# Kernel optimization log

Hardware: AMD Instinct MI355X
Metric: run time of the kernel (lower is better)

## Reference

```python
import jax, jax.numpy as jnp
import numpy as np

V, E, H, D = 30000, 300, 300, 300   # vocab, embed, enc_hid, dec_hid
B, TL, AL, QL = 128, 400, 50, 32    # batch, text_len, answer_len, question_len


def setup_inputs() -> dict:
    key = jax.random.key(0)
    ks = iter(jax.random.split(key, 40))
    def p(shape):
        return jax.random.normal(next(ks), shape, jnp.float32) * 0.05
    inp = {
        'text': jax.random.randint(next(ks), (B, TL), 0, V),
        'answer': jax.random.randint(next(ks), (B, AL), 0, V),
        'question': jax.random.randint(next(ks), (B, QL), 0, V),
        'embedding': p((V, E)),
        # text encoder (bidirectional GRU), torch gate order r,z,n
        'te_Wih_f': p((E, 3 * H)), 'te_Whh_f': p((H, 3 * H)), 'te_bih_f': p((3 * H,)), 'te_bhh_f': p((3 * H,)),
        'te_Wih_b': p((E, 3 * H)), 'te_Whh_b': p((H, 3 * H)), 'te_bih_b': p((3 * H,)), 'te_bhh_b': p((3 * H,)),
        # answer encoder (bidirectional GRU)
        'ae_Wih_f': p((E, 3 * H)), 'ae_Whh_f': p((H, 3 * H)), 'ae_bih_f': p((3 * H,)), 'ae_bhh_f': p((3 * H,)),
        'ae_Wih_b': p((E, 3 * H)), 'ae_Whh_b': p((H, 3 * H)), 'ae_bih_b': p((3 * H,)), 'ae_bhh_b': p((3 * H,)),
        'trans_W': p((2 * H, D)), 'trans_b': p((D,)),
        # attention: Linear(2H+D, D) split into key(D) and query(2H) blocks (cat order: key, queries)
        'attn_Wk': p((D, D)), 'attn_Wq': p((2 * H, D)), 'attn_b': p((D,)),
        'attn_v': jax.random.uniform(next(ks), (D,), jnp.float32),
        # decoder GRU cell, input = [emb(E), weighted(2H)]
        'dec_Wih': p((E + 2 * H, 3 * D)), 'dec_Whh': p((D, 3 * D)), 'dec_bih': p((3 * D,)), 'dec_bhh': p((3 * D,)),
        'out_W': p((D + 2 * H + E, V)), 'out_b': p((V,)),
    }
    return inp


def gru_cell(x, h, Wih, Whh, bih, bhh):
    gi = x @ Wih + bih
    gh = h @ Whh + bhh
    ir, iz, inn = jnp.split(gi, 3, axis=-1)
    hr, hz, hn = jnp.split(gh, 3, axis=-1)
    r = jax.nn.sigmoid(ir + hr)
    z = jax.nn.sigmoid(iz + hz)
    n = jnp.tanh(inn + r * hn)
    return (1 - z) * n + z * h


def gru_seq(x, Wih, Whh, bih, bhh, reverse=False):
    # x: [B,T,in] -> [B,T,H]
    xt = jnp.swapaxes(x, 0, 1)
    h0 = jnp.zeros((x.shape[0], Whh.shape[0]), x.dtype)
    def step(h, xt_):
        h = gru_cell(xt_, h, Wih, Whh, bih, bhh)
        return h, h
    _, ys = jax.lax.scan(step, h0, xt, reverse=reverse)
    return jnp.swapaxes(ys, 0, 1)


def bigru(x, Wih_f, Whh_f, bih_f, bhh_f, Wih_b, Whh_b, bih_b, bhh_b):
    fwd = gru_seq(x, Wih_f, Whh_f, bih_f, bhh_f, reverse=False)
    bwd = gru_seq(x, Wih_b, Whh_b, bih_b, bhh_b, reverse=True)
    return jnp.concatenate([fwd, bwd], axis=-1)  # [B,T,2H]


def reference(text, answer, question, embedding,
              te_Wih_f, te_Whh_f, te_bih_f, te_bhh_f, te_Wih_b, te_Whh_b, te_bih_b, te_bhh_b,
              ae_Wih_f, ae_Whh_f, ae_bih_f, ae_bhh_f, ae_Wih_b, ae_Whh_b, ae_bih_b, ae_bhh_b,
              trans_W, trans_b, attn_Wk, attn_Wq, attn_b, attn_v,
              dec_Wih, dec_Whh, dec_bih, dec_bhh, out_W, out_b):
    text_emb = embedding[text]          # [B,TL,E] (eval: dropout off)
    ans_emb = embedding[answer]
    q_emb = embedding[question]         # [B,QL,E]

    text_rep = bigru(text_emb, te_Wih_f, te_Whh_f, te_bih_f, te_bhh_f,
                     te_Wih_b, te_Whh_b, te_bih_b, te_bhh_b)      # [B,TL,2H]
    ans_rep = bigru(ans_emb, ae_Wih_f, ae_Whh_f, ae_bih_f, ae_bhh_f,
                    ae_Wih_b, ae_Whh_b, ae_bih_b, ae_bhh_b)       # [B,AL,2H]

    hidden0 = ans_rep[:, -1, :] @ trans_W + trans_b               # [B,D]
    # precompute query projection of attention (invariant over decode steps)
    qproj = jnp.einsum('bse,ed->bsd', text_rep, attn_Wq) + attn_b  # [B,TL,D]

    def step(h, emb_t):  # emb_t: [B,E]
        energy = jnp.tanh(qproj + (h @ attn_Wk)[:, None, :])      # [B,TL,D]
        scores = jnp.einsum('bsd,d->bs', energy, attn_v)
        a = jax.nn.softmax(scores, axis=1)
        weighted = jnp.einsum('bs,bse->be', a, text_rep)           # [B,2H]
        rnn_in = jnp.concatenate([emb_t, weighted], axis=-1)
        h_new = gru_cell(rnn_in, h, dec_Wih, dec_Whh, dec_bih, dec_bhh)
        logits = jnp.concatenate([h_new, weighted, emb_t], axis=-1) @ out_W + out_b
        return h_new, logits

    emb_seq = jnp.swapaxes(q_emb[:, :-1], 0, 1)  # teacher forcing: input at t is question[t-1]
    _, logits = jax.lax.scan(step, hidden0, emb_seq)   # [QL-1,B,V]
    logits = jnp.swapaxes(logits, 0, 1)                # [B,QL-1,V]
    outputs = jnp.concatenate([jnp.zeros((logits.shape[0], 1, logits.shape[2]), logits.dtype), logits], axis=1)
    return outputs  # [B,QL,V]
```

## Files before the change

### kernel.cpp

```cpp
#include <hip/hip_runtime.h>
#include <hip/hip_bf16.h>
#include <stdint.h>

typedef unsigned short u16;
typedef __attribute__((ext_vector_type(8))) short short8;
typedef __attribute__((ext_vector_type(4))) float f32x4;

#define B_   128
#define TL_  400
#define AL_  50
#define QL_  32
#define E_   300
#define H3_  900
#define V_   30000
#define EP_  320
#define K2P_ 640
#define KDP_ 1216
#define NDP_ 1920
#define MT_  51200
#define MA_  6400
#define MD_  3968

static __device__ __forceinline__ float bf2f(u16 u) {
    union { float f; unsigned v; } c; c.v = ((unsigned)u) << 16; return c.f;
}
static __device__ __forceinline__ u16 f2bf(float f) {
    union { float f; unsigned v; } c; c.f = f;
    unsigned r = c.v + 0x7FFF + ((c.v >> 16) & 1);
    return (u16)(r >> 16);
}
static __device__ __forceinline__ float sigm(float x) { return 1.f / (1.f + __expf(-x)); }

__global__ __launch_bounds__(256) void transpose_cvt(const float* __restrict__ src, int K, int N,
                                                     u16* __restrict__ dst, int ldbt, int n0, int k0) {
    __shared__ float tile[32][33];
    int kb = blockIdx.x * 32, nb = blockIdx.y * 32;
    int tx = threadIdx.x & 31, ty = threadIdx.x >> 5;
    for (int i = ty; i < 32; i += 8) {
        int k = kb + i, n = nb + tx;
        tile[i][tx] = (k < K && n < N) ? src[(size_t)k * N + n] : 0.f;
    }
    __syncthreads();
    for (int i = ty; i < 32; i += 8) {
        int n = nb + i, k = kb + tx;
        if (n < N && k < K) dst[(size_t)(n0 + n) * ldbt + k0 + k] = f2bf(tile[tx][i]);
    }
}

__global__ __launch_bounds__(256) void build_dec_bias(const float* __restrict__ bih,
                                                      const float* __restrict__ bhh,
                                                      float* __restrict__ bias) {
    int i = blockIdx.x * 256 + threadIdx.x;
    if (i < 900) bias[i] = bih[i];
    else if (i < 1800) bias[i] = bhh[i - 900];
    else if (i < NDP_) bias[i] = 0.f;
}

__global__ __launch_bounds__(256) void gather_rows(const int* __restrict__ idx, const float* __restrict__ emb,
                                                   u16* __restrict__ dst, int ldd) {
    int r = blockIdx.x;
    int id = idx[r];
    const float* e = emb + (size_t)id * E_;
    for (int i = threadIdx.x; i < E_; i += 256) dst[(size_t)r * ldd + i] = f2bf(e[i]);
}

__global__ __launch_bounds__(256) void gather_q(const int* __restrict__ question, const float* __restrict__ emb,
                                                u16* __restrict__ A_dec, u16* __restrict__ A_out) {
    int r = blockIdx.x;
    int t = r >> 7, b = r & 127;
    int id = question[b * QL_ + t];
    const float* e = emb + (size_t)id * E_;
    for (int i = threadIdx.x; i < E_; i += 256) {
        u16 u = f2bf(e[i]);
        A_dec[(size_t)r * KDP_ + i] = u;
        A_out[(size_t)r * KDP_ + 900 + i] = u;
    }
}

template <int MODE>
__global__ __launch_bounds__(256) void gemm_bt(const u16* __restrict__ A, int lda,
                                               const u16* __restrict__ Bt, int ldb,
                                               void* __restrict__ Cv, int ldc, int Nreal,
                                               const float* __restrict__ bias, int Kpad) {
    __shared__ u16 lA[128 * 32];
    __shared__ u16 lB[128 * 32];
    const int tid = threadIdx.x;
    const int bn = blockIdx.x, bm = blockIdx.y;
    const long row0 = (long)bm * 128;
    const u16* Ab = A + row0 * lda;
    const u16* Bb = Bt + (long)bn * 128 * ldb;
    const int lane = tid & 63, wave = tid >> 6;
    const int wr = wave >> 1, wc = wave & 1;
    const int lr = lane & 15, ko = (lane >> 4) * 8;
    f32x4 acc[4][4] = {};

    for (int k0 = 0; k0 < Kpad; k0 += 32) {
#pragma unroll
        for (int i = 0; i < 2; ++i) {
            const int c = tid + 256 * i;
            const int e = c * 8;
            const int r = e >> 5, col = e & 31;
            __builtin_amdgcn_global_load_lds(
                (const __attribute__((address_space(1))) void*)(Ab + (long)r * lda + k0 + col),
                (__attribute__((address_space(3))) void*)(&lA[e]), 16, 0, 0);
            __builtin_amdgcn_global_load_lds(
                (const __attribute__((address_space(1))) void*)(Bb + (long)r * ldb + k0 + col),
                (__attribute__((address_space(3))) void*)(&lB[e]), 16, 0, 0);
        }
        __syncthreads();
        short8 af[4], bfr[4];
#pragma unroll
        for (int i = 0; i < 4; ++i) {
            af[i]  = *(const short8*)&lA[(wr * 64 + i * 16 + lr) * 32 + ko];
            bfr[i] = *(const short8*)&lB[(wc * 64 + i * 16 + lr) * 32 + ko];
        }
#pragma unroll
        for (int i = 0; i < 4; ++i)
#pragma unroll
            for (int j = 0; j < 4; ++j)
                acc[i][j] = __builtin_amdgcn_mfma_f32_16x16x32_bf16(af[i], bfr[j], acc[i][j], 0, 0, 0);
        __syncthreads();
    }

    const int r4 = (lane >> 4) * 4;
    const int cl = lane & 15;
#pragma unroll
    for (int i = 0; i < 4; ++i) {
#pragma unroll
        for (int j = 0; j < 4; ++j) {
            const int colg = bn * 128 + wc * 64 + j * 16 + cl;
            if (colg >= Nreal) continue;
            const float bv = bias ? bias[colg] : 0.f;
#pragma unroll
            for (int v = 0; v < 4; ++v) {
                const long rowg = row0 + wr * 64 + i * 16 + r4 + v;
                const float val = acc[i][j][v] + bv;
                if (MODE == 0) {
                    ((float*)Cv)[rowg * (long)ldc + colg] = val;
                } else if (MODE == 1) {
                    ((u16*)Cv)[rowg * (long)ldc + colg] = f2bf(val);
                } else {
                    const int tt = (int)(rowg >> 7), bb = (int)(rowg & 127);
                    ((float*)Cv)[((long)bb * QL_ + tt + 1) * (long)V_ + colg] = val;
                }
            }
        }
    }
}

__global__ __launch_bounds__(256) void enc_step(int t,
        const float* __restrict__ Whh_tf, const float* __restrict__ Whh_tb,
        const float* __restrict__ Whh_af, const float* __restrict__ Whh_ab,
        const float* __restrict__ bhh_tf, const float* __restrict__ bhh_tb,
        const float* __restrict__ bhh_af, const float* __restrict__ bhh_ab,
        const u16* __restrict__ gi_tf, const u16* __restrict__ gi_tb,
        const u16* __restrict__ gi_af, const u16* __restrict__ gi_ab,
        float* __restrict__ h_enc, u16* __restrict__ text_rep) {
    const int blk = blockIdx.x;
    const int task = blk / 80;
    const int bg = (blk % 80) / 5;
    const int jc = blk % 5;
    if (task == 2 && t >= AL_) return;
    if (task == 3 && t != 0) return;
    const float* Whh; const float* bhh; const u16* gi; int T;
    if (task == 0)      { Whh = Whh_tf; bhh = bhh_tf; gi = gi_tf; T = TL_; }
    else if (task == 1) { Whh = Whh_tb; bhh = bhh_tb; gi = gi_tb; T = TL_; }
    else if (task == 2) { Whh = Whh_af; bhh = bhh_af; gi = gi_af; T = AL_; }
    else                { Whh = Whh_ab; bhh = bhh_ab; gi = gi_ab; T = AL_; }
    const int t_eff = (task == 1 || task == 3) ? (T - 1 - t) : t;

    __shared__ float hs[8 * 300];
    const float* h_cur = h_enc + (size_t)(((t & 1) * 4 + task) * 128 + bg * 8) * 300;
    float* h_nxt = h_enc + (size_t)((((t + 1) & 1) * 4 + task) * 128) * 300;
    const int tid = threadIdx.x;
    for (int i = tid; i < 2400; i += 256) hs[i] = h_cur[i];
    __syncthreads();

    const int j = jc * 64 + (tid & 63);
    if (j >= 300) return;
    const int bs = tid >> 6;
    float a0r = 0, a0z = 0, a0n = 0, a1r = 0, a1z = 0, a1n = 0;
    for (int k = 0; k < 300; ++k) {
        const float* wrow = Whh + k * 900;
        const float w0 = wrow[j], w1 = wrow[j + 300], w2 = wrow[j + 600];
        const float h0 = hs[bs * 300 + k], h1 = hs[(bs + 4) * 300 + k];
        a0r += h0 * w0; a0z += h0 * w1; a0n += h0 * w2;
        a1r += h1 * w0; a1z += h1 * w1; a1n += h1 * w2;
    }
    const float br = bhh[j], bz = bhh[j + 300], bnn = bhh[j + 600];
#pragma unroll
    for (int half = 0; half < 2; ++half) {
        const int bl = bs + half * 4;
        const int b = bg * 8 + bl;
        const float gr_ = half ? a1r : a0r, gz_ = half ? a1z : a0z, gn_ = half ? a1n : a0n;
        const size_t gidx = ((size_t)b * T + t_eff) * 900;
        const float gir = bf2f(gi[gidx + j]);
        const float giz = bf2f(gi[gidx + j + 300]);
        const float gin = bf2f(gi[gidx + j + 600]);
        const float r = sigm(gir + gr_ + br);
        const float z = sigm(giz + gz_ + bz);
        const float n = tanhf(gin + r * (gn_ + bnn));
        const float hp = hs[bl * 300 + j];
        const float hn = (1.f - z) * n + z * hp;
        h_nxt[(size_t)b * 300 + j] = hn;
        if (task < 2) text_rep[((size_t)b * TL_ + t_eff) * K2P_ + task * 300 + j] = f2bf(hn);
    }
}

__global__ __launch_bounds__(256) void trans_hidden(const float* __restrict__ h_enc,
                                                    const float* __restrict__ trans_W,
                                                    const float* __restrict__ trans_b,
                                                    float* __restrict__ h_dec, u16* __restrict__ A_dec0) {
    int b = blockIdx.x, tid = threadIdx.x;
    __shared__ float si[600];
    const float* af = h_enc + (size_t)((0 * 4 + 2) * 128 + b) * 300;
    const float* ab = h_enc + (size_t)((1 * 4 + 3) * 128 + b) * 300;
    for (int i = tid; i < 300; i += 256) { si[i] = af[i]; si[300 + i] = ab[i]; }
    __syncthreads();
    for (int jj = tid; jj < 300; jj += 256) {
        float acc = trans_b[jj];
        for (int k = 0; k < 600; ++k) acc += si[k] * trans_W[k * 300 + jj];
        h_dec[(size_t)b * 300 + jj] = acc;
        A_dec0[(size_t)b * KDP_ + 900 + jj] = f2bf(acc);
    }
}

__global__ __launch_bounds__(256) void attn_step(int t, const float* __restrict__ h_dec,
                                                 const float* __restrict__ Wk, const float* __restrict__ av,
                                                 const float* __restrict__ qproj, const u16* __restrict__ text_rep,
                                                 u16* __restrict__ A_dec_t, u16* __restrict__ A_out) {
    const int b = blockIdx.x, tid = threadIdx.x, lane = tid & 63, wave = tid >> 6;
    __shared__ float sh[300], hwk[300], sc[400], red[8];
    for (int i = tid; i < 300; i += 256) sh[i] = h_dec[(size_t)b * 300 + i];
    __syncthreads();
    for (int jj = tid; jj < 300; jj += 256) {
        float acc = 0.f;
        for (int k = 0; k < 300; ++k) acc += sh[k] * Wk[k * 300 + jj];
        hwk[jj] = acc;
    }
    __syncthreads();
    for (int s = wave; s < 400; s += 4) {
        const float* qp = qproj + ((size_t)b * TL_ + s) * 300;
        float p = 0.f;
        for (int d = lane; d < 300; d += 64) {
            float e = qp[d] + hwk[d];
            e = fminf(fmaxf(e, -15.f), 15.f);
            float ex = __expf(2.f * e);
            p += ((ex - 1.f) / (ex + 1.f)) * av[d];
        }
#pragma unroll
        for (int off = 32; off > 0; off >>= 1) p += __shfl_down(p, off);
        if (lane == 0) sc[s] = p;
    }
    __syncthreads();
    float m = -1e30f;
    for (int i = tid; i < 400; i += 256) m = fmaxf(m, sc[i]);
#pragma unroll
    for (int off = 32; off > 0; off >>= 1) m = fmaxf(m, __shfl_down(m, off));
    if (lane == 0) red[wave] = m;
    __syncthreads();
    m = fmaxf(fmaxf(red[0], red[1]), fmaxf(red[2], red[3]));
    float ssum = 0.f;
    for (int i = tid; i < 400; i += 256) { float e = __expf(sc[i] - m); sc[i] = e; ssum += e; }
#pragma unroll
    for (int off = 32; off > 0; off >>= 1) ssum += __shfl_down(ssum, off);
    if (lane == 0) red[4 + wave] = ssum;
    __syncthreads();
    const float inv = 1.f / (red[4] + red[5] + red[6] + red[7]);
    for (int e0 = tid; e0 < 600; e0 += 256) {
        float acc = 0.f;
        for (int s = 0; s < 400; ++s) acc += sc[s] * bf2f(text_rep[((size_t)b * TL_ + s) * K2P_ + e0]);
        u16 wv = f2bf(acc * inv);
        A_dec_t[(size_t)b * KDP_ + 300 + e0] = wv;
        A_out[((size_t)t * 128 + b) * KDP_ + 300 + e0] = wv;
    }
}

__global__ __launch_bounds__(256) void dec_gate(int t, const float* __restrict__ g_all,
                                                float* __restrict__ h_dec,
                                                u16* __restrict__ A_dec, u16* __restrict__ A_out) {
    int idx = blockIdx.x * 256 + threadIdx.x;
    if (idx >= 128 * 300) return;
    int b = idx / 300, j = idx % 300;
    const float* g = g_all + (size_t)b * NDP_;
    float r = sigm(g[j] + g[900 + j]);
    float z = sigm(g[300 + j] + g[1200 + j]);
    float n = tanhf(g[600 + j] + r * g[1500 + j]);
    float hp = h_dec[idx];
    float hn = (1.f - z) * n + z * hp;
    h_dec[idx] = hn;
    u16 u = f2bf(hn);
    A_out[((size_t)t * 128 + b) * KDP_ + j] = u;
    if (t < 30) A_dec[((size_t)(t + 1) * 128 + b) * KDP_ + 900 + j] = u;
}

__global__ __launch_bounds__(256) void zero_t0(float* __restrict__ out) {
    int i = blockIdx.x * 256 + threadIdx.x;
    if (i < 128 * V_) {
        int b = i / V_, v = i % V_;
        out[(size_t)b * QL_ * V_ + v] = 0.f;
    }
}

extern "C" void kernel_launch(void* const* d_in, const int* in_sizes, int n_in,
                              void* d_out, int out_size, void* d_ws, size_t ws_size,
                              hipStream_t stream) {
    (void)in_sizes; (void)n_in; (void)out_size;
    const int*   text      = (const int*)d_in[0];
    const int*   answer    = (const int*)d_in[1];
    const int*   question  = (const int*)d_in[2];
    const float* embedding = (const float*)d_in[3];
    const float* te_Wih_f = (const float*)d_in[4],  *te_Whh_f = (const float*)d_in[5];
    const float* te_bih_f = (const float*)d_in[6],  *te_bhh_f = (const float*)d_in[7];
    const float* te_Wih_b = (const float*)d_in[8],  *te_Whh_b = (const float*)d_in[9];
    const float* te_bih_b = (const float*)d_in[10], *te_bhh_b = (const float*)d_in[11];
    const float* ae_Wih_f = (const float*)d_in[12], *ae_Whh_f = (const float*)d_in[13];
    const float* ae_bih_f = (const float*)d_in[14], *ae_bhh_f = (const float*)d_in[15];
    const float* ae_Wih_b = (const float*)d_in[16], *ae_Whh_b = (const float*)d_in[17];
    const float* ae_bih_b = (const float*)d_in[18], *ae_bhh_b = (const float*)d_in[19];
    const float* trans_W  = (const float*)d_in[20], *trans_b  = (const float*)d_in[21];
    const float* attn_Wk  = (const float*)d_in[22], *attn_Wq  = (const float*)d_in[23];
    const float* attn_b   = (const float*)d_in[24], *attn_v   = (const float*)d_in[25];
    const float* dec_Wih  = (const float*)d_in[26], *dec_Whh  = (const float*)d_in[27];
    const float* dec_bih  = (const float*)d_in[28], *dec_bhh  = (const float*)d_in[29];
    const float* out_W    = (const float*)d_in[30], *out_b    = (const float*)d_in[31];
    float* out = (float*)d_out;

    char* w = (char*)d_ws; size_t off = 0;
    auto alloc = [&](size_t bytes) -> void* { void* p = w + off; off += (bytes + 255) & ~(size_t)255; return p; };
    u16* WihT_tf = (u16*)alloc(1024 * EP_ * 2);
    u16* WihT_tb = (u16*)alloc(1024 * EP_ * 2);
    u16* WihT_af = (u16*)alloc(1024 * EP_ * 2);
    u16* WihT_ab = (u16*)alloc(1024 * EP_ * 2);
    u16* WqT     = (u16*)alloc(384 * K2P_ * 2);
    u16* outWT   = (u16*)alloc((size_t)30080 * KDP_ * 2);
    u16* decBT   = (u16*)alloc((size_t)NDP_ * KDP_ * 2);
    float* decBias = (float*)alloc(NDP_ * 4);
    u16* textEmb = (u16*)alloc((size_t)MT_ * EP_ * 2);
    u16* ansEmb  = (u16*)alloc((size_t)MA_ * EP_ * 2);
    u16* gi_tf   = (u16*)alloc((size_t)MT_ * 900 * 2);
    u16* gi_tb   = (u16*)alloc((size_t)MT_ * 900 * 2);
    u16* gi_af   = (u16*)alloc((size_t)MA_ * 900 * 2);
    u16* gi_ab   = (u16*)alloc((size_t)MA_ * 900 * 2);
    u16* text_rep = (u16*)alloc((size_t)MT_ * K2P_ * 2);
    float* qproj = (float*)alloc((size_t)MT_ * 300 * 4);
    float* h_enc = (float*)alloc((size_t)2 * 4 * 128 * 300 * 4);
    float* h_dec = (float*)alloc((size_t)128 * 300 * 4);
    u16* A_dec   = (u16*)alloc((size_t)MD_ * KDP_ * 2);
    u16* A_out   = (u16*)alloc((size_t)MD_ * KDP_ * 2);
    float* gi_gh = (float*)alloc((size_t)128 * NDP_ * 4);
    const size_t need = off;
    size_t zbytes = need <= ws_size ? need : ws_size;

    hipMemsetAsync(d_ws, 0, zbytes, stream);

    transpose_cvt<<<dim3(10, 29), 256, 0, stream>>>(te_Wih_f, 300, 900, WihT_tf, EP_, 0, 0);
    transpose_cvt<<<dim3(10, 29), 256, 0, stream>>>(te_Wih_b, 300, 900, WihT_tb, EP_, 0, 0);
    transpose_cvt<<<dim3(10, 29), 256, 0, stream>>>(ae_Wih_f, 300, 900, WihT_af, EP_, 0, 0);
    transpose_cvt<<<dim3(10, 29), 256, 0, stream>>>(ae_Wih_b, 300, 900, WihT_ab, EP_, 0, 0);
    transpose_cvt<<<dim3(19, 10), 256, 0, stream>>>(attn_Wq, 600, 300, WqT, K2P_, 0, 0);
    transpose_cvt<<<dim3(38, 938), 256, 0, stream>>>(out_W, 1200, V_, outWT, KDP_, 0, 0);
    transpose_cvt<<<dim3(29, 29), 256, 0, stream>>>(dec_Wih, 900, 900, decBT, KDP_, 0, 0);
    transpose_cvt<<<dim3(10, 29), 256, 0, stream>>>(dec_Whh, 300, 900, decBT, KDP_, 900, 900);
    build_dec_bias<<<8, 256, 0, stream>>>(dec_bih, dec_bhh, decBias);

    gather_rows<<<MT_, 256, 0, stream>>>(text, embedding, textEmb, EP_);
    gather_rows<<<MA_, 256, 0, stream>>>(answer, embedding, ansEmb, EP_);
    gather_q<<<MD_, 256, 0, stream>>>(question, embedding, A_dec, A_out);

    gemm_bt<1><<<dim3(8, 400), 256, 0, stream>>>(textEmb, EP_, WihT_tf, EP_, gi_tf, 900, 900, te_bih_f, EP_);
    gemm_bt<1><<<dim3(8, 400), 256, 0, stream>>>(textEmb, EP_, WihT_tb, EP_, gi_tb, 900, 900, te_bih_b, EP_);
    gemm_bt<1><<<dim3(8, 50),  256, 0, stream>>>(ansEmb, EP_, WihT_af, EP_, gi_af, 900, 900, ae_bih_f, EP_);
    gemm_bt<1><<<dim3(8, 50),  256, 0, stream>>>(ansEmb, EP_, WihT_ab, EP_, gi_ab, 900, 900, ae_bih_b, EP_);

    for (int t = 0; t < TL_; ++t)
        enc_step<<<320, 256, 0, stream>>>(t, te_Whh_f, te_Whh_b, ae_Whh_f, ae_Whh_b,
                                          te_bhh_f, te_bhh_b, ae_bhh_f, ae_bhh_b,
                                          gi_tf, gi_tb, gi_af, gi_ab, h_enc, text_rep);

    trans_hidden<<<128, 256, 0, stream>>>(h_enc, trans_W, trans_b, h_dec, A_dec);
    gemm_bt<0><<<dim3(3, 400), 256, 0, stream>>>(text_rep, K2P_, WqT, K2P_, qproj, 300, 300, attn_b, K2P_);

    for (int t = 0; t < QL_ - 1; ++t) {
        attn_step<<<128, 256, 0, stream>>>(t, h_dec, attn_Wk, attn_v, qproj, text_rep,
                                           A_dec + (size_t)t * 128 * KDP_, A_out);
        gemm_bt<0><<<dim3(15, 1), 256, 0, stream>>>(A_dec + (size_t)t * 128 * KDP_, KDP_,
                                                    decBT, KDP_, gi_gh, NDP_, 1800, decBias, KDP_);
        dec_gate<<<150, 256, 0, stream>>>(t, gi_gh, h_dec, A_dec, A_out);
    }

    gemm_bt<2><<<dim3(235, 31), 256, 0, stream>>>(A_out, KDP_, outWT, KDP_, d_out, 0, V_, out_b, KDP_);
    zero_t0<<<(128 * V_ + 255) / 256, 256, 0, stream>>>(out);
}
```

Before: 18.73 ms.

## Replace per-step encoder GRU launches with persistent MFMA kernel over time

```diff
diff --git a/kernel.cpp b/kernel.cpp
--- a/kernel.cpp
+++ b/kernel.cpp
@@ -4,6 +4,7 @@
 
 typedef unsigned short u16;
 typedef __attribute__((ext_vector_type(8))) short short8;
+typedef __attribute__((ext_vector_type(8))) _Float16 half8;
 typedef __attribute__((ext_vector_type(4))) float f32x4;
 
 #define B_   128
@@ -11,7 +12,6 @@
 #define AL_  50
 #define QL_  32
 #define E_   300
-#define H3_  900
 #define V_   30000
 #define EP_  320
 #define K2P_ 640
@@ -20,6 +20,7 @@
 #define MT_  51200
 #define MA_  6400
 #define MD_  3968
+#define WPT_ (10*1024*32)
 
 static __device__ __forceinline__ float bf2f(u16 u) {
     union { float f; unsigned v; } c; c.v = ((unsigned)u) << 16; return c.f;
@@ -28,6 +29,9 @@
     union { float f; unsigned v; } c; c.f = f;
     unsigned r = c.v + 0x7FFF + ((c.v >> 16) & 1);
     return (u16)(r >> 16);
+}
+static __device__ __forceinline__ u16 f2h_bits(float f) {
+    _Float16 h = (_Float16)f; u16 u; __builtin_memcpy(&u, &h, 2); return u;
 }
 static __device__ __forceinline__ float sigm(float x) { return 1.f / (1.f + __expf(-x)); }
 
@@ -45,6 +49,26 @@
         int n = nb + i, k = kb + tx;
         if (n < N && k < K) dst[(size_t)(n0 + n) * ldbt + k0 + k] = f2bf(tile[tx][i]);
     }
+}
+
+__global__ __launch_bounds__(320) void prep_whh(const float* __restrict__ W0, const float* __restrict__ W1,
+                                                const float* __restrict__ W2, const float* __restrict__ W3,
+                                                const float* __restrict__ b0, const float* __restrict__ b1,
+                                                const float* __restrict__ b2, const float* __restrict__ b3,
+                                                u16* __restrict__ dst) {
+    int c = blockIdx.x, task = blockIdx.y;
+    const float* W = task == 0 ? W0 : task == 1 ? W1 : task == 2 ? W2 : W3;
+    const float* b = task == 0 ? b0 : task == 1 ? b1 : task == 2 ? b2 : b3;
+    int k = threadIdx.x;
+    float val = 0.f;
+    if (c < 912) {
+        int g = c / 304, j = c % 304;
+        if (j < 300) {
+            if (k < 300) val = W[(size_t)k * 900 + g * 300 + j];
+            else if (k == 300) val = b[g * 300 + j];
+        }
+    }
+    dst[(size_t)task * WPT_ + ((size_t)(k >> 5) * 1024 + c) * 32 + (k & 31)] = f2h_bits(val);
 }
 
 __global__ __launch_bounds__(256) void build_dec_bias(const float* __restrict__ bih,
@@ -148,73 +172,124 @@
     }
 }
 
-__global__ __launch_bounds__(256) void enc_step(int t,
-        const float* __restrict__ Whh_tf, const float* __restrict__ Whh_tb,
-        const float* __restrict__ Whh_af, const float* __restrict__ Whh_ab,
-        const float* __restrict__ bhh_tf, const float* __restrict__ bhh_tb,
-        const float* __restrict__ bhh_af, const float* __restrict__ bhh_ab,
+__global__ __launch_bounds__(512) void enc_persist(
+        const u16* __restrict__ Wp_all,
         const u16* __restrict__ gi_tf, const u16* __restrict__ gi_tb,
         const u16* __restrict__ gi_af, const u16* __restrict__ gi_ab,
-        float* __restrict__ h_enc, u16* __restrict__ text_rep) {
-    const int blk = blockIdx.x;
-    const int task = blk / 80;
-    const int bg = (blk % 80) / 5;
-    const int jc = blk % 5;
-    if (task == 2 && t >= AL_) return;
-    if (task == 3 && t != 0) return;
-    const float* Whh; const float* bhh; const u16* gi; int T;
-    if (task == 0)      { Whh = Whh_tf; bhh = bhh_tf; gi = gi_tf; T = TL_; }
-    else if (task == 1) { Whh = Whh_tb; bhh = bhh_tb; gi = gi_tb; T = TL_; }
-    else if (task == 2) { Whh = Whh_af; bhh = bhh_af; gi = gi_af; T = AL_; }
-    else                { Whh = Whh_ab; bhh = bhh_ab; gi = gi_ab; T = AL_; }
-    const int t_eff = (task == 1 || task == 3) ? (T - 1 - t) : t;
-
-    __shared__ float hs[8 * 300];
-    const float* h_cur = h_enc + (size_t)(((t & 1) * 4 + task) * 128 + bg * 8) * 300;
-    float* h_nxt = h_enc + (size_t)((((t + 1) & 1) * 4 + task) * 128) * 300;
-    const int tid = threadIdx.x;
-    for (int i = tid; i < 2400; i += 256) hs[i] = h_cur[i];
-    __syncthreads();
-
-    const int j = jc * 64 + (tid & 63);
-    if (j >= 300) return;
-    const int bs = tid >> 6;
-    float a0r = 0, a0z = 0, a0n = 0, a1r = 0, a1z = 0, a1n = 0;
-    for (int k = 0; k < 300; ++k) {
-        const float* wrow = Whh + k * 900;
-        const float w0 = wrow[j], w1 = wrow[j + 300], w2 = wrow[j + 600];
-        const float h0 = hs[bs * 300 + k], h1 = hs[(bs + 4) * 300 + k];
-        a0r += h0 * w0; a0z += h0 * w1; a0n += h0 * w2;
-        a1r += h1 * w0; a1z += h1 * w1; a1n += h1 * w2;
-    }
-    const float br = bhh[j], bz = bhh[j + 300], bnn = bhh[j + 600];
-#pragma unroll
-    for (int half = 0; half < 2; ++half) {
-        const int bl = bs + half * 4;
-        const int b = bg * 8 + bl;
-        const float gr_ = half ? a1r : a0r, gz_ = half ? a1z : a0z, gn_ = half ? a1n : a0n;
-        const size_t gidx = ((size_t)b * T + t_eff) * 900;
-        const float gir = bf2f(gi[gidx + j]);
-        const float giz = bf2f(gi[gidx + j + 300]);
-        const float gin = bf2f(gi[gidx + j + 600]);
-        const float r = sigm(gir + gr_ + br);
-        const float z = sigm(giz + gz_ + bz);
-        const float n = tanhf(gin + r * (gn_ + bnn));
-        const float hp = hs[bl * 300 + j];
-        const float hn = (1.f - z) * n + z * hp;
-        h_nxt[(size_t)b * 300 + j] = hn;
-        if (task < 2) text_rep[((size_t)b * TL_ + t_eff) * K2P_ + task * 300 + j] = f2bf(hn);
-    }
-}
-
-__global__ __launch_bounds__(256) void trans_hidden(const float* __restrict__ h_enc,
+        u16* __restrict__ text_rep, float* __restrict__ h_fin) {
+    const int task = blockIdx.x >> 2, bslice = blockIdx.x & 3;
+    const u16* Wp = Wp_all + (size_t)task * WPT_;
+    const u16* gi; int T, Tloop, rev;
+    if (task == 0)      { gi = gi_tf; T = 400; Tloop = 400; rev = 0; }
+    else if (task == 1) { gi = gi_tb; T = 400; Tloop = 400; rev = 1; }
+    else if (task == 2) { gi = gi_af; T = 50;  Tloop = 50;  rev = 0; }
+    else                { gi = gi_ab; T = 50;  Tloop = 1;   rev = 1; }
+
+    __shared__ u16 bT[1024 * 32];
+    __shared__ u16 hHi[10 * 32 * 32];
+    __shared__ u16 hLo[10 * 32 * 32];
+
+    const int tid = threadIdx.x, lane = tid & 63, wave = tid >> 6;
+    const int wm = wave >> 2, wn = wave & 3;
+    const int lr = lane & 15, ko8 = (lane >> 4) * 8;
+    const int q = lane >> 4, jl = lane & 15;
+
+    for (int i = tid; i < 10240; i += 512) { hHi[i] = 0; hLo[i] = 0; }
+    __syncthreads();
+    if (tid < 32) hHi[(9 * 32 + tid) * 32 + 12] = 0x3C00;
+    __syncthreads();
+
+    float hprev[20];
+#pragma unroll
+    for (int i = 0; i < 20; ++i) hprev[i] = 0.f;
+
+    for (int t = 0; t < Tloop; ++t) {
+        const int te = rev ? (T - 1 - t) : t;
+        f32x4 acc[15] = {};
+        for (int kt = 0; kt < 10; ++kt) {
+#pragma unroll
+            for (int r = 0; r < 8; ++r) {
+                int idx = r * 512 + tid;
+                __builtin_amdgcn_global_load_lds(
+                    (const __attribute__((address_space(1))) void*)(Wp + (size_t)kt * 32768 + idx * 8),
+                    (__attribute__((address_space(3))) void*)(&bT[idx * 8]), 16, 0, 0);
+            }
+            __syncthreads();
+            half8 afh = *(const half8*)&hHi[((kt * 32) + wm * 16 + lr) * 32 + ko8];
+            half8 afl = *(const half8*)&hLo[((kt * 32) + wm * 16 + lr) * 32 + ko8];
+#pragma unroll
+            for (int gx = 0; gx < 5; ++gx) {
+                const int G = wn + 4 * gx;
+                if (G < 19) {
+#pragma unroll
+                    for (int gate = 0; gate < 3; ++gate) {
+                        const int tn = 19 * gate + G;
+                        half8 bf = *(const half8*)&bT[(tn * 16 + lr) * 32 + ko8];
+                        acc[gx * 3 + gate] = __builtin_amdgcn_mfma_f32_16x16x32_f16(afh, bf, acc[gx * 3 + gate], 0, 0, 0);
+                        acc[gx * 3 + gate] = __builtin_amdgcn_mfma_f32_16x16x32_f16(afl, bf, acc[gx * 3 + gate], 0, 0, 0);
+                    }
+                }
+            }
+            __syncthreads();
+        }
+#pragma unroll
+        for (int gx = 0; gx < 5; ++gx) {
+            const int G = wn + 4 * gx;
+            if (G >= 19) continue;
+            const int j = G * 16 + jl;
+            if (j >= 300) continue;
+#pragma unroll
+            for (int v = 0; v < 4; ++v) {
+                const int batch = wm * 16 + q * 4 + v;
+                const int bglob = bslice * 32 + batch;
+                const u16* gp = gi + ((size_t)bglob * T + te) * 900;
+                const float ar = acc[gx * 3 + 0][v];
+                const float az = acc[gx * 3 + 1][v];
+                const float an = acc[gx * 3 + 2][v];
+                float r_ = sigm(bf2f(gp[j]) + ar);
+                float z_ = sigm(bf2f(gp[j + 300]) + az);
+                float x = bf2f(gp[j + 600]) + r_ * an;
+                x = fminf(fmaxf(x, -15.f), 15.f);
+                float e = __expf(2.f * x);
+                float n_ = (e - 1.f) / (e + 1.f);
+                float hn = (1.f - z_) * n_ + z_ * hprev[gx * 4 + v];
+                hprev[gx * 4 + v] = hn;
+                _Float16 hh = (_Float16)hn;
+                float hhf = (float)hh;
+                _Float16 hl = (_Float16)(hn - hhf);
+                u16 uhh, uhl;
+                __builtin_memcpy(&uhh, &hh, 2);
+                __builtin_memcpy(&uhl, &hl, 2);
+                const int hidx = ((j >> 5) * 32 + batch) * 32 + (j & 31);
+                hHi[hidx] = uhh;
+                hLo[hidx] = uhl;
+                if (task < 2) text_rep[((size_t)bglob * TL_ + te) * K2P_ + task * 300 + j] = f2bf(hn);
+            }
+        }
+        __syncthreads();
+    }
+    if (task >= 2) {
+#pragma unroll
+        for (int gx = 0; gx < 5; ++gx) {
+            const int G = wn + 4 * gx; if (G >= 19) continue;
+            const int j = G * 16 + jl; if (j >= 300) continue;
+#pragma unroll
+            for (int v = 0; v < 4; ++v) {
+                const int bglob = bslice * 32 + wm * 16 + q * 4 + v;
+                h_fin[(size_t)(task - 2) * 38400 + (size_t)bglob * 300 + j] = hprev[gx * 4 + v];
+            }
+        }
+    }
+}
+
+__global__ __launch_bounds__(256) void trans_hidden(const float* __restrict__ h_fin,
                                                     const float* __restrict__ trans_W,
                                                     const float* __restrict__ trans_b,
                                                     float* __restrict__ h_dec, u16* __restrict__ A_dec0) {
     int b = blockIdx.x, tid = threadIdx.x;
     __shared__ float si[600];
-    const float* af = h_enc + (size_t)((0 * 4 + 2) * 128 + b) * 300;
-    const float* ab = h_enc + (size_t)((1 * 4 + 3) * 128 + b) * 300;
+    const float* af = h_fin + (size_t)b * 300;
+    const float* ab = h_fin + 38400 + (size_t)b * 300;
     for (int i = tid; i < 300; i += 256) { si[i] = af[i]; si[300 + i] = ab[i]; }
     __syncthreads();
     for (int jj = tid; jj < 300; jj += 256) {
@@ -336,6 +411,7 @@
     u16* outWT   = (u16*)alloc((size_t)30080 * KDP_ * 2);
     u16* decBT   = (u16*)alloc((size_t)NDP_ * KDP_ * 2);
     float* decBias = (float*)alloc(NDP_ * 4);
+    u16* WhhPt   = (u16*)alloc((size_t)4 * WPT_ * 2);
     u16* textEmb = (u16*)alloc((size_t)MT_ * EP_ * 2);
     u16* ansEmb  = (u16*)alloc((size_t)MA_ * EP_ * 2);
     u16* gi_tf   = (u16*)alloc((size_t)MT_ * 900 * 2);
@@ -344,7 +420,7 @@
     u16* gi_ab   = (u16*)alloc((size_t)MA_ * 900 * 2);
     u16* text_rep = (u16*)alloc((size_t)MT_ * K2P_ * 2);
     float* qproj = (float*)alloc((size_t)MT_ * 300 * 4);
-    float* h_enc = (float*)alloc((size_t)2 * 4 * 128 * 300 * 4);
+    float* h_fin = (float*)alloc((size_t)2 * 128 * 300 * 4);
     float* h_dec = (float*)alloc((size_t)128 * 300 * 4);
     u16* A_dec   = (u16*)alloc((size_t)MD_ * KDP_ * 2);
     u16* A_out   = (u16*)alloc((size_t)MD_ * KDP_ * 2);
@@ -358,6 +434,8 @@
     transpose_cvt<<<dim3(10, 29), 256, 0, stream>>>(te_Wih_b, 300, 900, WihT_tb, EP_, 0, 0);
     transpose_cvt<<<dim3(10, 29), 256, 0, stream>>>(ae_Wih_f, 300, 900, WihT_af, EP_, 0, 0);
     transpose_cvt<<<dim3(10, 29), 256, 0, stream>>>(ae_Wih_b, 300, 900, WihT_ab, EP_, 0, 0);
+    prep_whh<<<dim3(1024, 4), 320, 0, stream>>>(te_Whh_f, te_Whh_b, ae_Whh_f, ae_Whh_b,
+                                                te_bhh_f, te_bhh_b, ae_bhh_f, ae_bhh_b, WhhPt);
     transpose_cvt<<<dim3(19, 10), 256, 0, stream>>>(attn_Wq, 600, 300, WqT, K2P_, 0, 0);
     transpose_cvt<<<dim3(38, 938), 256, 0, stream>>>(out_W, 1200, V_, outWT, KDP_, 0, 0);
     transpose_cvt<<<dim3(29, 29), 256, 0, stream>>>(dec_Wih, 900, 900, decBT, KDP_, 0, 0);
@@ -373,12 +451,9 @@
     gemm_bt<1><<<dim3(8, 50),  256, 0, stream>>>(ansEmb, EP_, WihT_af, EP_, gi_af, 900, 900, ae_bih_f, EP_);
     gemm_bt<1><<<dim3(8, 50),  256, 0, stream>>>(ansEmb, EP_, WihT_ab, EP_, gi_ab, 900, 900, ae_bih_b, EP_);
 
-    for (int t = 0; t < TL_; ++t)
-        enc_step<<<320, 256, 0, stream>>>(t, te_Whh_f, te_Whh_b, ae_Whh_f, ae_Whh_b,
-                                          te_bhh_f, te_bhh_b, ae_bhh_f, ae_bhh_b,
-                                          gi_tf, gi_tb, gi_af, gi_ab, h_enc, text_rep);
-
-    trans_hidden<<<128, 256, 0, stream>>>(h_enc, trans_W, trans_b, h_dec, A_dec);
+    enc_persist<<<16, 512, 0, stream>>>(WhhPt, gi_tf, gi_tb, gi_af, gi_ab, text_rep, h_fin);
+
+    trans_hidden<<<128, 256, 0, stream>>>(h_fin, trans_W, trans_b, h_dec, A_dec);
     gemm_bt<0><<<dim3(3, 400), 256, 0, stream>>>(text_rep, K2P_, WqT, K2P_, qproj, 300, 300, attn_b, K2P_);
 
     for (int t = 0; t < QL_ - 1; ++t) {
```

Measured after the change: 28.26 ms. +50.9%, slower.
